# Kernel optimization log

Measured on AMD Instinct MI355X. Metric: run time of the kernel, lower is better.

The kernel has to match this reference:

```python
import jax, jax.numpy as jnp
import numpy as np
from jax import lax

EPS = 1e-6

def _ln(z, w, b):
    # torch F.layer_norm over last dim, biased variance
    mu = z.mean(-1, keepdims=True)
    v = ((z - mu) ** 2).mean(-1, keepdims=True)
    return (z - mu) / jnp.sqrt(v + EPS) * w + b

def setup_inputs() -> dict:
    key = jax.random.key(0)
    ks = jax.random.split(key, 8)
    B, C, H, W = 128, 384, 28, 28
    N = H * W
    nkeep = N // 2  # ratio 0.5
    x = jax.random.normal(ks[0], (B, C, H, W), dtype=jnp.float32)
    # routing indices: per-batch permutation split (as argsort of scores in PredictorLG)
    score = jax.random.normal(ks[1], (B, N), dtype=jnp.float32)
    idx = jnp.argsort(score, axis=1)[:, ::-1].astype(jnp.int32)
    idx1 = idx[:, :nkeep]
    idx2 = idx[:, nkeep:]
    dw_w = jax.random.normal(ks[2], (C, 1, 7, 7), dtype=jnp.float32) * 0.05
    dw_b = jnp.zeros((C,), jnp.float32)
    norm_w = jnp.ones((C,), jnp.float32)
    norm_b = jnp.zeros((C,), jnp.float32)
    w1 = jax.random.normal(ks[3], (C, 4 * C), dtype=jnp.float32) * 0.02
    b1 = jnp.zeros((4 * C,), jnp.float32)
    w2 = jax.random.normal(ks[4], (4 * C, C), dtype=jnp.float32) * 0.02
    b2 = jnp.zeros((C,), jnp.float32)
    gamma = jnp.full((C,), 1e-6, jnp.float32)
    fp_norm_w = jnp.ones((C,), jnp.float32)
    fp_norm_b = jnp.zeros((C,), jnp.float32)
    fp_w = jax.random.normal(ks[5], (C, C), dtype=jnp.float32) * 0.02
    fp_b = jnp.zeros((C,), jnp.float32)
    fp_gamma = jnp.full((C,), 1e-6, jnp.float32)
    return dict(x=x, idx1=idx1, idx2=idx2, dw_w=dw_w, dw_b=dw_b, norm_w=norm_w,
                norm_b=norm_b, w1=w1, b1=b1, w2=w2, b2=b2, gamma=gamma,
                fp_norm_w=fp_norm_w, fp_norm_b=fp_norm_b, fp_w=fp_w, fp_b=fp_b,
                fp_gamma=fp_gamma)

def reference(x, idx1, idx2, dw_w, dw_b, norm_w, norm_b, w1, b1, w2, b2,
              gamma, fp_norm_w, fp_norm_b, fp_w, fp_b, fp_gamma):
    B, C, H, W = x.shape
    N = H * W
    # depthwise 7x7 conv, padding 3
    y = lax.conv_general_dilated(x, dw_w, (1, 1), [(3, 3), (3, 3)],
                                 feature_group_count=C,
                                 dimension_numbers=('NCHW', 'OIHW', 'NCHW'))
    y = y + dw_b[None, :, None, None]
    t = y.transpose(0, 2, 3, 1).reshape(B, N, C)  # (B, N, C)
    # gather tokens for each branch
    x1 = jnp.take_along_axis(t, idx1[..., None].astype(jnp.int32), axis=1)  # (B, N1, C)
    x2 = jnp.take_along_axis(t, idx2[..., None].astype(jnp.int32), axis=1)  # (B, N2, C)
    # full FFN branch
    h = _ln(x1, norm_w, norm_b) @ w1 + b1
    h = jax.nn.gelu(h, approximate=False)
    x1 = (h @ w2 + b2) * gamma
    # fast path branch
    x2 = (_ln(x2, fp_norm_w, fp_norm_b) @ fp_w + fp_b) * fp_gamma
    # scatter-merge back
    out = jnp.zeros_like(t)
    bi = jnp.arange(B)[:, None]
    out = out.at[bi, idx1].set(x1).at[bi, idx2].set(x2)
    out = out.reshape(B, H, W, C).transpose(0, 3, 1, 2)
    return x + out
```

## Files before the change

### kernel.cpp

```cpp
#include <hip/hip_runtime.h>
#include <hip/hip_fp8.h>
#include <math.h>

typedef unsigned short u16;
typedef unsigned char u8;
typedef short s16x8 __attribute__((ext_vector_type(8)));
typedef short s16x4 __attribute__((ext_vector_type(4)));
typedef unsigned int u32x4 __attribute__((ext_vector_type(4)));
typedef unsigned int u32x2 __attribute__((ext_vector_type(2)));
typedef __bf16 bf16x8 __attribute__((ext_vector_type(8)));
typedef float f32x4 __attribute__((ext_vector_type(4)));
typedef unsigned short u16x2 __attribute__((ext_vector_type(2)));

__device__ __forceinline__ float bf2f(u16 u) {
  unsigned x = ((unsigned)u) << 16;
  return __builtin_bit_cast(float, x);
}
__device__ __forceinline__ u16 f2bf(float f) {
  unsigned x = __builtin_bit_cast(unsigned, f);
  unsigned r = (x + 0x7FFFu + ((x >> 16) & 1u)) >> 16;
  return (u16)r;
}
__device__ __forceinline__ u8 f2e4(float f) {
  __hip_fp8_e4m3 q(f);
  return (u8)q.__x;
}
__device__ __forceinline__ unsigned cvt2e4(float a, float b) {
#if __has_builtin(__builtin_amdgcn_cvt_pk_fp8_f32)
  return (unsigned)__builtin_amdgcn_cvt_pk_fp8_f32(a, b, 0, false) & 0xFFFFu;
#else
  return (unsigned)f2e4(a) | ((unsigned)f2e4(b) << 8);
#endif
}

__device__ __forceinline__ f32x4 mfma8(long a, long b, f32x4 c) {
  return __builtin_amdgcn_mfma_f32_16x16x32_fp8_fp8(a, b, c, 0, 0, 0);
}

__device__ __forceinline__ void gload_lds16(const u16* g, u16* l) {
  __builtin_amdgcn_global_load_lds(
      (__attribute__((address_space(1))) void*)(u16*)g,
      (__attribute__((address_space(3))) void*)l, 16, 0, 0);
}

__global__ __launch_bounds__(256) void pack_kernel(
    const float* __restrict__ w1, const float* __restrict__ w2,
    const float* __restrict__ fpw, const int* __restrict__ idx1,
    const int* __restrict__ idx2, u8* __restrict__ w1p8, u8* __restrict__ w2p8,
    u8* __restrict__ fpw8, int* __restrict__ rm1, int* __restrict__ rm2) {
  const int T1 = 589824;
  const int T2 = T1 + 589824;
  const int T3 = T2 + 147456;
  const int T4 = T3 + 50176;
  const int T5 = T4 + 50176;
  int stride = gridDim.x * 256;
  for (int i = blockIdx.x * 256 + threadIdx.x; i < T5; i += stride) {
    if (i < T1) {
      int k = i / 1536, n = i - k * 1536;
      w1p8[((size_t)(k >> 3) * 1536 + n) * 8 + (k & 7)] = f2e4(w1[i] * 64.f);
    } else if (i < T2) {
      int t = i - T1;
      int k = t / 384, n = t - k * 384;
      w2p8[((size_t)(k >> 3) * 384 + n) * 8 + (k & 7)] = f2e4(w2[t] * 64.f);
    } else if (i < T3) {
      int t = i - T2;
      int k = t / 384, n = t - k * 384;
      fpw8[((size_t)(k >> 3) * 384 + n) * 8 + (k & 7)] = f2e4(fpw[t] * 64.f);
    } else if (i < T4) {
      int g = i - T3;
      rm1[g] = (g / 392) * 784 + idx1[g];
    } else {
      int g = i - T4;
      rm2[g] = (g / 392) * 784 + idx2[g];
    }
  }
}

__global__ __launch_bounds__(256) void dwconv_kernel(
    const float* __restrict__ x, const float* __restrict__ dww,
    const float* __restrict__ dwb, u16* __restrict__ t) {
  __shared__ __align__(16) u16 plane[8 * 34 * 40];
  int tid = threadIdx.x;
  int b = blockIdx.y, c0 = blockIdx.x * 8;
  int ch = tid & 7, row = tid >> 3;
  int c = c0 + ch;

  float wg[49];
#pragma unroll
  for (int k2 = 0; k2 < 49; ++k2) wg[k2] = dww[c * 49 + k2];
  float bias = dwb[c];

  for (int q = tid; q < 1360; q += 256) {
    s16x8 z = {0, 0, 0, 0, 0, 0, 0, 0};
    *(s16x8*)(&plane[q * 8]) = z;
  }
  __syncthreads();
  for (int q = tid; q < 1568; q += 256) {
    int cc = q / 196, seg = q - cc * 196;
    int i = seg / 7, j4 = seg - i * 7;
    const float4 v = *(const float4*)(x + ((size_t)(b * 384 + c0 + cc)) * 784 +
                                      i * 28 + j4 * 4);
    s16x4 p;
    p[0] = (short)f2bf(v.x);
    p[1] = (short)f2bf(v.y);
    p[2] = (short)f2bf(v.z);
    p[3] = (short)f2bf(v.w);
    *(s16x4*)(&plane[cc * 1360 + (3 + i) * 40 + 4 + j4 * 4]) = p;
  }
  __syncthreads();

  if (row < 28) {
    size_t obase = ((size_t)(b * 784 + row * 28)) * 384 + c;
#pragma unroll
    for (int ck = 0; ck < 4; ++ck) {
      float acc[8];
#pragma unroll
      for (int o = 0; o < 8; ++o) acc[o] = bias;
#pragma unroll
      for (int di = 0; di < 7; ++di) {
        const u16* base2 = &plane[ch * 1360 + (row + di) * 40 + ck * 8];
        u32x4 ga = *(const u32x4*)(base2);
        u32x4 gb = *(const u32x4*)(base2 + 8);
        unsigned dw[8] = {ga[0], ga[1], ga[2], ga[3],
                          gb[0], gb[1], gb[2], gb[3]};
        float v[16];
#pragma unroll
        for (int tt = 0; tt < 16; ++tt) {
          unsigned d = dw[tt >> 1];
          v[tt] = (tt & 1) ? __builtin_bit_cast(float, d & 0xFFFF0000u)
                           : __builtin_bit_cast(float, d << 16);
        }
#pragma unroll
        for (int o = 0; o < 8; ++o)
#pragma unroll
          for (int dj = 0; dj < 7; ++dj)
            acc[o] += v[o + dj + 1] * wg[di * 7 + dj];
      }
      int lim = (ck == 3) ? 4 : 8;
#pragma unroll
      for (int o = 0; o < 8; ++o)
        if (o < lim) t[obase + (size_t)(ck * 8 + o) * 384] = f2bf(acc[o]);
    }
  }
}

__global__ __launch_bounds__(256) void gatherln_kernel(
    const u16* __restrict__ t, const int* __restrict__ idx1,
    const int* __restrict__ idx2, const float* __restrict__ nw1,
    const float* __restrict__ nb1, const float* __restrict__ nw2,
    const float* __restrict__ nb2, u8* __restrict__ A1f,
    u8* __restrict__ A2f) {
  int wid = threadIdx.x >> 6, lane = threadIdx.x & 63;
  int g = blockIdx.x * 4 + wid;
  bool is1 = g < 50176;
  int gg = is1 ? g : g - 50176;
  const int* idx = is1 ? idx1 : idx2;
  int b = gg / 392;
  int jj = gg - b * 392;
  int ntok = idx[b * 392 + jj];
  const u16* src = t + ((size_t)(b * 784 + ntok)) * 384 + lane * 6;
  float v[6];
  u16x2 u0 = *(const u16x2*)(src);
  u16x2 u1 = *(const u16x2*)(src + 2);
  u16x2 u2 = *(const u16x2*)(src + 4);
  v[0] = bf2f(u0[0]); v[1] = bf2f(u0[1]);
  v[2] = bf2f(u1[0]); v[3] = bf2f(u1[1]);
  v[4] = bf2f(u2[0]); v[5] = bf2f(u2[1]);
  float s = 0.f, q = 0.f;
#pragma unroll
  for (int e = 0; e < 6; ++e) { s += v[e]; q += v[e] * v[e]; }
#pragma unroll
  for (int off = 32; off >= 1; off >>= 1) {
    s += __shfl_xor(s, off);
    q += __shfl_xor(q, off);
  }
  float mu = s * (1.f / 384.f);
  float var = q * (1.f / 384.f) - mu * mu;
  float rs = rsqrtf(var + 1e-6f);
  const float* nw = is1 ? nw1 : nw2;
  const float* nb = is1 ? nb1 : nb2;
  int k0 = lane * 6;
  float o[6];
#pragma unroll
  for (int e = 0; e < 6; ++e)
    o[e] = (v[e] - mu) * rs * nw[k0 + e] + nb[k0 + e];
  u8* dst = (is1 ? A1f : A2f) + (size_t)gg * 384 + lane * 6;
#pragma unroll
  for (int e = 0; e < 6; e += 2) *(u16*)(dst + e) = (u16)cvt2e4(o[e], o[e + 1]);
}

__global__ __launch_bounds__(256, 4) void fused_mlp_kernel(
    const u8* __restrict__ A, const u8* __restrict__ w1p8,
    const u8* __restrict__ w2p8, const float* __restrict__ b1,
    const float* __restrict__ b2, const float* __restrict__ gamma,
    const int* __restrict__ rm, u16* __restrict__ U) {
  __shared__ __align__(16) u8 Alds[48 * 32 * 8];
  __shared__ __align__(16) u8 Plds[2][24 * 32 * 8];
  int tid = threadIdx.x;
  int wid = tid >> 6, lane = tid & 63;
  int kgl = lane >> 4, rl = lane & 15;
  int cl = lane & 15, rg = (lane >> 4) * 4;
  int m_base = blockIdx.x * 32;

#pragma unroll
  for (int it = 0; it < 3; ++it) {
    int c16 = it * 256 + tid;
    int row = c16 / 24, cc = c16 - row * 24;
    u32x4 v = *(const u32x4*)(A + (size_t)(m_base + row) * 384 + cc * 16);
    u32x2 lo = {v[0], v[1]}, hi = {v[2], v[3]};
    *(u32x2*)&Alds[((2 * cc) * 32 + row) * 8] = lo;
    *(u32x2*)&Alds[((2 * cc + 1) * 32 + row) * 8] = hi;
  }

  const f32x4 vzero = {0.f, 0.f, 0.f, 0.f};
  f32x4 accB[2][6];
#pragma unroll
  for (int i = 0; i < 2; ++i)
#pragma unroll
    for (int j = 0; j < 6; ++j) accB[i][j] = vzero;

  __syncthreads();

#pragma unroll 1
  for (int c = 0; c < 8; ++c) {
    u8* Pl = Plds[c & 1];
    f32x4 accA[2][3];
#pragma unroll
    for (int i = 0; i < 2; ++i)
#pragma unroll
      for (int j = 0; j < 3; ++j) accA[i][j] = vzero;
#pragma unroll
    for (int ks = 0; ks < 12; ++ks) {
      long af[2], bw[3];
#pragma unroll
      for (int i = 0; i < 2; ++i)
        af[i] = *(const long*)&Alds[((ks * 4 + kgl) * 32 + i * 16 + rl) * 8];
#pragma unroll
      for (int j = 0; j < 3; ++j) {
        int col = c * 192 + wid * 48 + j * 16 + rl;
        bw[j] = *(const long*)(w1p8 + ((size_t)(ks * 4 + kgl) * 1536 + col) * 8);
      }
      __builtin_amdgcn_s_setprio(1);
#pragma unroll
      for (int i = 0; i < 2; ++i)
#pragma unroll
        for (int j = 0; j < 3; ++j)
          accA[i][j] = mfma8(af[i], bw[j], accA[i][j]);
      __builtin_amdgcn_s_setprio(0);
    }
    float b1v[3];
#pragma unroll
    for (int j = 0; j < 3; ++j) b1v[j] = b1[c * 192 + wid * 48 + j * 16 + cl];
#pragma unroll
    for (int i = 0; i < 2; ++i)
#pragma unroll
      for (int j = 0; j < 3; ++j) {
        int col = wid * 48 + j * 16 + cl;
        float g2[4];
#pragma unroll
        for (int reg = 0; reg < 4; ++reg) {
          float v = accA[i][j][reg] * 0.015625f + b1v[j];
          g2[reg] = v * fminf(fmaxf(0.4255f * v + 0.5f, 0.f), 1.f);
        }
        unsigned p01 = cvt2e4(g2[0], g2[1]);
        unsigned p23 = cvt2e4(g2[2], g2[3]);
        int base = ((col >> 3) * 32 + i * 16 + rg) * 8 + (col & 7);
        Pl[base] = (u8)p01;
        Pl[base + 8] = (u8)(p01 >> 8);
        Pl[base + 16] = (u8)p23;
        Pl[base + 24] = (u8)(p23 >> 8);
      }
    __syncthreads();
#pragma unroll
    for (int ks = 0; ks < 6; ++ks) {
      long ap[2], bw2[6];
#pragma unroll
      for (int i = 0; i < 2; ++i)
        ap[i] = *(const long*)&Pl[((ks * 4 + kgl) * 32 + i * 16 + rl) * 8];
#pragma unroll
      for (int j = 0; j < 6; ++j) {
        int col = wid * 96 + j * 16 + rl;
        int ko2 = c * 24 + ks * 4 + kgl;
        bw2[j] = *(const long*)(w2p8 + ((size_t)ko2 * 384 + col) * 8);
      }
      __builtin_amdgcn_s_setprio(1);
#pragma unroll
      for (int i = 0; i < 2; ++i)
#pragma unroll
        for (int j = 0; j < 6; ++j)
          accB[i][j] = mfma8(ap[i], bw2[j], accB[i][j]);
      __builtin_amdgcn_s_setprio(0);
    }
  }

#pragma unroll
  for (int i = 0; i < 2; ++i) {
#pragma unroll
    for (int reg = 0; reg < 4; ++reg) {
      int m = m_base + i * 16 + rg + reg;
      size_t rowoff = (size_t)rm[m] * 384;
#pragma unroll
      for (int j = 0; j < 6; ++j) {
        int col = wid * 96 + j * 16 + cl;
        float v = (accB[i][j][reg] * 0.015625f + b2[col]) * gamma[col];
        U[rowoff + col] = f2bf(v);
      }
    }
  }
}

__global__ __launch_bounds__(256, 4) void gemm5_kernel(
    const u8* __restrict__ A, const u8* __restrict__ wp8,
    const float* __restrict__ bias, const float* __restrict__ scale,
    const int* __restrict__ rm, u16* __restrict__ U) {
  __shared__ __align__(16) u8 Alds[48 * 32 * 8];
  int tid = threadIdx.x;
  int wid = tid >> 6, lane = tid & 63;
  int kgl = lane >> 4, rl = lane & 15;
  int cl = lane & 15, rg = (lane >> 4) * 4;
  int m_base = blockIdx.x * 32;

#pragma unroll
  for (int it = 0; it < 3; ++it) {
    int c16 = it * 256 + tid;
    int row = c16 / 24, cc = c16 - row * 24;
    u32x4 v = *(const u32x4*)(A + (size_t)(m_base + row) * 384 + cc * 16);
    u32x2 lo = {v[0], v[1]}, hi = {v[2], v[3]};
    *(u32x2*)&Alds[((2 * cc) * 32 + row) * 8] = lo;
    *(u32x2*)&Alds[((2 * cc + 1) * 32 + row) * 8] = hi;
  }

  const f32x4 vzero = {0.f, 0.f, 0.f, 0.f};
  f32x4 acc[2][6];
#pragma unroll
  for (int i = 0; i < 2; ++i)
#pragma unroll
    for (int j = 0; j < 6; ++j) acc[i][j] = vzero;

  __syncthreads();

#pragma unroll
  for (int ks = 0; ks < 12; ++ks) {
    long af[2], bw[6];
#pragma unroll
    for (int i = 0; i < 2; ++i)
      af[i] = *(const long*)&Alds[((ks * 4 + kgl) * 32 + i * 16 + rl) * 8];
#pragma unroll
    for (int j = 0; j < 6; ++j) {
      int col = wid * 96 + j * 16 + rl;
      bw[j] = *(const long*)(wp8 + ((size_t)(ks * 4 + kgl) * 384 + col) * 8);
    }
    __builtin_amdgcn_s_setprio(1);
#pragma unroll
    for (int i = 0; i < 2; ++i)
#pragma unroll
      for (int j = 0; j < 6; ++j)
        acc[i][j] = mfma8(af[i], bw[j], acc[i][j]);
    __builtin_amdgcn_s_setprio(0);
  }

#pragma unroll
  for (int i = 0; i < 2; ++i) {
#pragma unroll
    for (int reg = 0; reg < 4; ++reg) {
      int m = m_base + i * 16 + rg + reg;
      size_t rowoff = (size_t)rm[m] * 384;
#pragma unroll
      for (int j = 0; j < 6; ++j) {
        int col = wid * 96 + j * 16 + cl;
        float v = (acc[i][j][reg] * 0.015625f + bias[col]) * scale[col];
        U[rowoff + col] = f2bf(v);
      }
    }
  }
}

__global__ __launch_bounds__(256) void unscatter_add_kernel(
    const u16* __restrict__ U, const float* __restrict__ x,
    float* __restrict__ out) {
  __shared__ float tile[32][129];
  int b = blockIdx.y;
  int ct = blockIdx.x % 12, nt = blockIdx.x / 12;
  int c0 = ct * 32, n0 = nt * 128;
  int tid = threadIdx.x;
#pragma unroll
  for (int it = 0; it < 4; ++it) {
    int q = tid + it * 256;
    int nl = q >> 3, cg = (q & 7) * 4;
    int n = n0 + nl;
    if (n < 784) {
      s16x4 v = *(const s16x4*)(U + ((size_t)(b * 784 + n)) * 384 + c0 + cg);
      tile[cg + 0][nl] = bf2f((u16)v[0]);
      tile[cg + 1][nl] = bf2f((u16)v[1]);
      tile[cg + 2][nl] = bf2f((u16)v[2]);
      tile[cg + 3][nl] = bf2f((u16)v[3]);
    }
  }
  __syncthreads();
#pragma unroll
  for (int it = 0; it < 4; ++it) {
    int q = tid + it * 256;
    int c = q >> 5, nf = (q & 31) * 4;
    int n = n0 + nf;
    if (n + 3 < 784) {
      size_t o = ((size_t)(b * 384 + c0 + c)) * 784 + n;
      float4 xv = *(const float4*)(x + o);
      float4 r;
      r.x = xv.x + tile[c][nf + 0];
      r.y = xv.y + tile[c][nf + 1];
      r.z = xv.z + tile[c][nf + 2];
      r.w = xv.w + tile[c][nf + 3];
      *(float4*)(out + o) = r;
    }
  }
}

extern "C" void kernel_launch(void* const* d_in, const int* in_sizes, int n_in,
                              void* d_out, int out_size, void* d_ws,
                              size_t ws_size, hipStream_t stream) {
  const float* x = (const float*)d_in[0];
  const int* idx1 = (const int*)d_in[1];
  const int* idx2 = (const int*)d_in[2];
  const float* dww = (const float*)d_in[3];
  const float* dwb = (const float*)d_in[4];
  const float* nw = (const float*)d_in[5];
  const float* nb = (const float*)d_in[6];
  const float* w1 = (const float*)d_in[7];
  const float* b1 = (const float*)d_in[8];
  const float* w2 = (const float*)d_in[9];
  const float* b2 = (const float*)d_in[10];
  const float* gamma = (const float*)d_in[11];
  const float* fnw = (const float*)d_in[12];
  const float* fnb = (const float*)d_in[13];
  const float* fpw = (const float*)d_in[14];
  const float* fpb = (const float*)d_in[15];
  const float* fpg = (const float*)d_in[16];

  char* ws = (char*)d_ws;
  u16* t = (u16*)(ws);
  u8* A1f = (u8*)(ws + 77070336);
  u8* A2f = (u8*)(ws + 96337920);
  u16* U = (u16*)(ws + 115605504);
  u8* w1p8 = (u8*)(ws + 192675840);
  u8* w2p8 = (u8*)(ws + 193265664);
  u8* fpw8 = (u8*)(ws + 193855488);
  int* rm1 = (int*)(ws + 194002944);
  int* rm2 = (int*)(ws + 194203648);
  (void)ws_size; (void)in_sizes; (void)n_in; (void)out_size;

  pack_kernel<<<1024, 256, 0, stream>>>(w1, w2, fpw, idx1, idx2, w1p8, w2p8,
                                        fpw8, rm1, rm2);
  dwconv_kernel<<<dim3(48, 128), 256, 0, stream>>>(x, dww, dwb, t);
  gatherln_kernel<<<25088, 256, 0, stream>>>(t, idx1, idx2, nw, nb, fnw, fnb,
                                             A1f, A2f);
  fused_mlp_kernel<<<1568, 256, 0, stream>>>(A1f, w1p8, w2p8, b1, b2, gamma,
                                             rm1, U);
  gemm5_kernel<<<1568, 256, 0, stream>>>(A2f, fpw8, fpb, fpg, rm2, U);
  unscatter_add_kernel<<<dim3(84, 128), 256, 0, stream>>>(U, x,
                                                          (float*)d_out);
}
```

Baseline: 393.8 us.

## Fuse gather and LayerNorm into GEMM prologues, drop gatherln kernel

Removes the standalone gather+LayerNorm kernel. Each GEMM block now gathers its 32 token rows from the bf16 conv output via the row map, computes LayerNorm with an 8-lane reduction, quantizes to fp8, and writes straight into the LDS A-tile. This removes one launch and the round trip through the fp8 A1f/A2f intermediates in global memory, and shrinks the workspace. In exchange, each GEMM block performs scattered bf16 row loads and the LayerNorm arithmetic before its MFMA loop starts.

```diff
diff --git a/kernel.cpp b/kernel.cpp
--- a/kernel.cpp
+++ b/kernel.cpp
@@ -8,7 +8,6 @@
 typedef short s16x4 __attribute__((ext_vector_type(4)));
 typedef unsigned int u32x4 __attribute__((ext_vector_type(4)));
 typedef unsigned int u32x2 __attribute__((ext_vector_type(2)));
-typedef __bf16 bf16x8 __attribute__((ext_vector_type(8)));
 typedef float f32x4 __attribute__((ext_vector_type(4)));
 typedef unsigned short u16x2 __attribute__((ext_vector_type(2)));
 
@@ -37,10 +36,55 @@
   return __builtin_amdgcn_mfma_f32_16x16x32_fp8_fp8(a, b, c, 0, 0, 0);
 }
 
-__device__ __forceinline__ void gload_lds16(const u16* g, u16* l) {
-  __builtin_amdgcn_global_load_lds(
-      (__attribute__((address_space(1))) void*)(u16*)g,
-      (__attribute__((address_space(3))) void*)l, 16, 0, 0);
+__device__ __forceinline__ void stage_ln(
+    const u16* __restrict__ t, const int* __restrict__ rm, int m_base,
+    const float* __restrict__ nw, const float* __restrict__ nb, u8* Alds,
+    int tid) {
+  int row = tid >> 3, seg = tid & 7;
+  const u16* src = t + (size_t)rm[m_base + row] * 384 + seg * 48;
+  u32x4 raw[6];
+#pragma unroll
+  for (int o = 0; o < 6; ++o) raw[o] = *(const u32x4*)(src + o * 8);
+  float s = 0.f, q = 0.f;
+#pragma unroll
+  for (int o = 0; o < 6; ++o)
+#pragma unroll
+    for (int w = 0; w < 4; ++w) {
+      unsigned d = raw[o][w];
+      float lo = bf2f((u16)(d & 0xFFFFu));
+      float hi = bf2f((u16)(d >> 16));
+      s += lo + hi;
+      q += lo * lo + hi * hi;
+    }
+#pragma unroll
+  for (int off = 1; off <= 4; off <<= 1) {
+    s += __shfl_xor(s, off);
+    q += __shfl_xor(q, off);
+  }
+  float mu = s * (1.f / 384.f);
+  float var = q * (1.f / 384.f) - mu * mu;
+  float rs = rsqrtf(var + 1e-6f);
+#pragma unroll
+  for (int o = 0; o < 6; ++o) {
+    int k0 = seg * 48 + o * 8;
+    float4 w0 = *(const float4*)(nw + k0);
+    float4 w1 = *(const float4*)(nw + k0 + 4);
+    float4 c0 = *(const float4*)(nb + k0);
+    float4 c1 = *(const float4*)(nb + k0 + 4);
+    unsigned d0 = raw[o][0], d1 = raw[o][1], d2 = raw[o][2], d3 = raw[o][3];
+    float g0 = (bf2f((u16)(d0 & 0xFFFFu)) - mu) * rs * w0.x + c0.x;
+    float g1 = (bf2f((u16)(d0 >> 16)) - mu) * rs * w0.y + c0.y;
+    float g2 = (bf2f((u16)(d1 & 0xFFFFu)) - mu) * rs * w0.z + c0.z;
+    float g3 = (bf2f((u16)(d1 >> 16)) - mu) * rs * w0.w + c0.w;
+    float g4 = (bf2f((u16)(d2 & 0xFFFFu)) - mu) * rs * w1.x + c1.x;
+    float g5 = (bf2f((u16)(d2 >> 16)) - mu) * rs * w1.y + c1.y;
+    float g6 = (bf2f((u16)(d3 & 0xFFFFu)) - mu) * rs * w1.z + c1.z;
+    float g7 = (bf2f((u16)(d3 >> 16)) - mu) * rs * w1.w + c1.w;
+    u32x2 pk;
+    pk[0] = cvt2e4(g0, g1) | (cvt2e4(g2, g3) << 16);
+    pk[1] = cvt2e4(g4, g5) | (cvt2e4(g6, g7) << 16);
+    *(u32x2*)&Alds[((seg * 6 + o) * 32 + row) * 8] = pk;
+  }
 }
 
 __global__ __launch_bounds__(256) void pack_kernel(
@@ -144,56 +188,12 @@
   }
 }
 
-__global__ __launch_bounds__(256) void gatherln_kernel(
-    const u16* __restrict__ t, const int* __restrict__ idx1,
-    const int* __restrict__ idx2, const float* __restrict__ nw1,
-    const float* __restrict__ nb1, const float* __restrict__ nw2,
-    const float* __restrict__ nb2, u8* __restrict__ A1f,
-    u8* __restrict__ A2f) {
-  int wid = threadIdx.x >> 6, lane = threadIdx.x & 63;
-  int g = blockIdx.x * 4 + wid;
-  bool is1 = g < 50176;
-  int gg = is1 ? g : g - 50176;
-  const int* idx = is1 ? idx1 : idx2;
-  int b = gg / 392;
-  int jj = gg - b * 392;
-  int ntok = idx[b * 392 + jj];
-  const u16* src = t + ((size_t)(b * 784 + ntok)) * 384 + lane * 6;
-  float v[6];
-  u16x2 u0 = *(const u16x2*)(src);
-  u16x2 u1 = *(const u16x2*)(src + 2);
-  u16x2 u2 = *(const u16x2*)(src + 4);
-  v[0] = bf2f(u0[0]); v[1] = bf2f(u0[1]);
-  v[2] = bf2f(u1[0]); v[3] = bf2f(u1[1]);
-  v[4] = bf2f(u2[0]); v[5] = bf2f(u2[1]);
-  float s = 0.f, q = 0.f;
-#pragma unroll
-  for (int e = 0; e < 6; ++e) { s += v[e]; q += v[e] * v[e]; }
-#pragma unroll
-  for (int off = 32; off >= 1; off >>= 1) {
-    s += __shfl_xor(s, off);
-    q += __shfl_xor(q, off);
-  }
-  float mu = s * (1.f / 384.f);
-  float var = q * (1.f / 384.f) - mu * mu;
-  float rs = rsqrtf(var + 1e-6f);
-  const float* nw = is1 ? nw1 : nw2;
-  const float* nb = is1 ? nb1 : nb2;
-  int k0 = lane * 6;
-  float o[6];
-#pragma unroll
-  for (int e = 0; e < 6; ++e)
-    o[e] = (v[e] - mu) * rs * nw[k0 + e] + nb[k0 + e];
-  u8* dst = (is1 ? A1f : A2f) + (size_t)gg * 384 + lane * 6;
-#pragma unroll
-  for (int e = 0; e < 6; e += 2) *(u16*)(dst + e) = (u16)cvt2e4(o[e], o[e + 1]);
-}
-
 __global__ __launch_bounds__(256, 4) void fused_mlp_kernel(
-    const u8* __restrict__ A, const u8* __restrict__ w1p8,
-    const u8* __restrict__ w2p8, const float* __restrict__ b1,
-    const float* __restrict__ b2, const float* __restrict__ gamma,
-    const int* __restrict__ rm, u16* __restrict__ U) {
+    const u16* __restrict__ t, const int* __restrict__ rm,
+    const float* __restrict__ nw, const float* __restrict__ nb,
+    const u8* __restrict__ w1p8, const u8* __restrict__ w2p8,
+    const float* __restrict__ b1, const float* __restrict__ b2,
+    const float* __restrict__ gamma, u16* __restrict__ U) {
   __shared__ __align__(16) u8 Alds[48 * 32 * 8];
   __shared__ __align__(16) u8 Plds[2][24 * 32 * 8];
   int tid = threadIdx.x;
@@ -202,15 +202,7 @@
   int cl = lane & 15, rg = (lane >> 4) * 4;
   int m_base = blockIdx.x * 32;
 
-#pragma unroll
-  for (int it = 0; it < 3; ++it) {
-    int c16 = it * 256 + tid;
-    int row = c16 / 24, cc = c16 - row * 24;
-    u32x4 v = *(const u32x4*)(A + (size_t)(m_base + row) * 384 + cc * 16);
-    u32x2 lo = {v[0], v[1]}, hi = {v[2], v[3]};
-    *(u32x2*)&Alds[((2 * cc) * 32 + row) * 8] = lo;
-    *(u32x2*)&Alds[((2 * cc + 1) * 32 + row) * 8] = hi;
-  }
+  stage_ln(t, rm, m_base, nw, nb, Alds, tid);
 
   const f32x4 vzero = {0.f, 0.f, 0.f, 0.f};
   f32x4 accB[2][6];
@@ -310,9 +302,10 @@
 }
 
 __global__ __launch_bounds__(256, 4) void gemm5_kernel(
-    const u8* __restrict__ A, const u8* __restrict__ wp8,
-    const float* __restrict__ bias, const float* __restrict__ scale,
-    const int* __restrict__ rm, u16* __restrict__ U) {
+    const u16* __restrict__ t, const int* __restrict__ rm,
+    const float* __restrict__ nw, const float* __restrict__ nb,
+    const u8* __restrict__ wp8, const float* __restrict__ bias,
+    const float* __restrict__ scale, u16* __restrict__ U) {
   __shared__ __align__(16) u8 Alds[48 * 32 * 8];
   int tid = threadIdx.x;
   int wid = tid >> 6, lane = tid & 63;
@@ -320,15 +313,7 @@
   int cl = lane & 15, rg = (lane >> 4) * 4;
   int m_base = blockIdx.x * 32;
 
-#pragma unroll
-  for (int it = 0; it < 3; ++it) {
-    int c16 = it * 256 + tid;
-    int row = c16 / 24, cc = c16 - row * 24;
-    u32x4 v = *(const u32x4*)(A + (size_t)(m_base + row) * 384 + cc * 16);
-    u32x2 lo = {v[0], v[1]}, hi = {v[2], v[3]};
-    *(u32x2*)&Alds[((2 * cc) * 32 + row) * 8] = lo;
-    *(u32x2*)&Alds[((2 * cc + 1) * 32 + row) * 8] = hi;
-  }
+  stage_ln(t, rm, m_base, nw, nb, Alds, tid);
 
   const f32x4 vzero = {0.f, 0.f, 0.f, 0.f};
   f32x4 acc[2][6];
@@ -438,24 +423,20 @@
 
   char* ws = (char*)d_ws;
   u16* t = (u16*)(ws);
-  u8* A1f = (u8*)(ws + 77070336);
-  u8* A2f = (u8*)(ws + 96337920);
-  u16* U = (u16*)(ws + 115605504);
-  u8* w1p8 = (u8*)(ws + 192675840);
-  u8* w2p8 = (u8*)(ws + 193265664);
-  u8* fpw8 = (u8*)(ws + 193855488);
-  int* rm1 = (int*)(ws + 194002944);
-  int* rm2 = (int*)(ws + 194203648);
+  u16* U = (u16*)(ws + 77070336);
+  u8* w1p8 = (u8*)(ws + 154140672);
+  u8* w2p8 = (u8*)(ws + 154730496);
+  u8* fpw8 = (u8*)(ws + 155320320);
+  int* rm1 = (int*)(ws + 155467776);
+  int* rm2 = (int*)(ws + 155668480);
   (void)ws_size; (void)in_sizes; (void)n_in; (void)out_size;
 
   pack_kernel<<<1024, 256, 0, stream>>>(w1, w2, fpw, idx1, idx2, w1p8, w2p8,
                                         fpw8, rm1, rm2);
   dwconv_kernel<<<dim3(48, 128), 256, 0, stream>>>(x, dww, dwb, t);
-  gatherln_kernel<<<25088, 256, 0, stream>>>(t, idx1, idx2, nw, nb, fnw, fnb,
-                                             A1f, A2f);
-  fused_mlp_kernel<<<1568, 256, 0, stream>>>(A1f, w1p8, w2p8, b1, b2, gamma,
-                                             rm1, U);
-  gemm5_kernel<<<1568, 256, 0, stream>>>(A2f, fpw8, fpb, fpg, rm2, U);
+  fused_mlp_kernel<<<1568, 256, 0, stream>>>(t, rm1, nw, nb, w1p8, w2p8, b1,
+                                             b2, gamma, U);
+  gemm5_kernel<<<1568, 256, 0, stream>>>(t, rm2, fnw, fnb, fpw8, fpb, fpg, U);
   unscatter_add_kernel<<<dim3(84, 128), 256, 0, stream>>>(U, x,
                                                           (float*)d_out);
 }
```

Result: no change. 387.6 us (-1.6%).
